# Performance work log

Hardware: AMD Instinct MI355X
Metric: run time of the kernel (lower is better)

## Reference

```python
import jax, jax.numpy as jnp
import numpy as np

S, B, E, H = 2048, 2, 1024, 16
D = E // H  # head_dim = 64


def setup_inputs() -> dict:
    key = jax.random.key(0)
    ks = jax.random.split(key, 5)
    sp = (2.0 / (E + E)) ** 0.5  # xavier-ish scale
    return {
        "x": jax.random.normal(ks[0], (S, B, E), dtype=jnp.float32),
        "wq": jax.random.normal(ks[1], (E, E), dtype=jnp.float32) * sp,
        "bq": jnp.zeros((E,), jnp.float32),
        "wk": jax.random.normal(ks[2], (E, E), dtype=jnp.float32) * sp,
        "bk": jnp.zeros((E,), jnp.float32),
        "wv": jax.random.normal(ks[3], (E, E), dtype=jnp.float32) * sp,
        "bv": jnp.zeros((E,), jnp.float32),
        "wo": jax.random.normal(ks[4], (E, E), dtype=jnp.float32) * sp,
        "bo": jnp.zeros((E,), jnp.float32),
    }


def reference(x, wq, bq, wk, bk, wv, bv, wo, bo):
    # x: (S, B, E), weights in torch Linear convention (out, in)
    scaling = jnp.float32(D ** -0.5)
    q = (jnp.einsum('ibe,fe->ibf', x, wq) + bq) * scaling
    k = jnp.einsum('ibe,fe->ibf', x, wk) + bk
    v = jnp.einsum('ibe,fe->ibf', x, wv) + bv
    q = q.reshape(S, B, H, D)
    k = k.reshape(S, B, H, D)
    v = v.reshape(S, B, H, D)
    # energy: (B, H, S_q, S_k)
    energy = jnp.einsum('ibnf,jbnf->bnij', q, k)
    causal = jnp.triu(jnp.ones((S, S), dtype=bool), k=1)  # True above diagonal
    energy = jnp.where(causal[None, None], -jnp.inf, energy)
    weights = jax.nn.softmax(energy, axis=-1)
    head_ctx = jnp.einsum('bnij,jbnf->ibnf', weights, v)
    context = head_ctx.reshape(S, B, E)
    out = jnp.einsum('ibe,fe->ibf', context, wo) + bo
    return out
```

## Files before the change

### kernel.cpp

```cpp
#include <hip/hip_runtime.h>
#include <hip/hip_bf16.h>
#include <stdint.h>

#define S_LEN 2048
#define BATCH 2
#define EMB   1024
#define NH    16
#define HD    64
#define LOG2E 1.4426950408889634f

typedef __bf16 bf16x8 __attribute__((ext_vector_type(8)));
typedef float  f32x4  __attribute__((ext_vector_type(4)));
typedef unsigned short ushort8 __attribute__((ext_vector_type(8)));

__device__ __forceinline__ unsigned short f2bf(float f) {
  __bf16 h = (__bf16)f;
  return __builtin_bit_cast(unsigned short, h);
}

__device__ __forceinline__ ushort8 cvt8(const float4 a, const float4 b) {
  ushort8 o;
  o[0]=f2bf(a.x); o[1]=f2bf(a.y); o[2]=f2bf(a.z); o[3]=f2bf(a.w);
  o[4]=f2bf(b.x); o[5]=f2bf(b.y); o[6]=f2bf(b.z); o[7]=f2bf(b.w);
  return o;
}

__device__ __forceinline__ uint2 pack4(const f32x4 v) {
  uint2 r;
  r.x = (unsigned)f2bf(v[0]) | ((unsigned)f2bf(v[1]) << 16);
  r.y = (unsigned)f2bf(v[2]) | ((unsigned)f2bf(v[3]) << 16);
  return r;
}

#define GLOAD16(g, l) __builtin_amdgcn_global_load_lds( \
    (const __attribute__((address_space(1))) void*)(g),  \
    (__attribute__((address_space(3))) void*)(l), 16, 0, 0)

__global__ __launch_bounds__(256) void k_cvt(const float* __restrict__ src,
                                             unsigned short* __restrict__ dst,
                                             int n) {
  int i = (blockIdx.x*256 + threadIdx.x)*8;
  if (i >= n) return;
  const float4* s4 = (const float4*)(src + i);
  *(ushort8*)(dst + i) = cvt8(s4[0], s4[1]);
}

__global__ __launch_bounds__(256) void k_cvt_all(
    const float* __restrict__ x,
    const float* __restrict__ wq, const float* __restrict__ wk,
    const float* __restrict__ wv, const float* __restrict__ wo,
    unsigned short* __restrict__ xb, unsigned short* __restrict__ wb,
    unsigned short* __restrict__ wob) {
  const int b = blockIdx.x;
  const float* src;
  unsigned short* dst;
  int off;
  if (b < 2048) { src = x; dst = xb; off = b; }
  else {
    const int t = b - 2048;
    const int z = t >> 9;
    if (z < 3) { src = (z==0) ? wq : ((z==1) ? wk : wv); dst = wb + (size_t)z*EMB*EMB; }
    else       { src = wo; dst = wob; }
    off = t & 511;
  }
  const int i = (off*256 + threadIdx.x)*8;
  const float4* s4 = (const float4*)(src + i);
  *(ushort8*)(dst + i) = cvt8(s4[0], s4[1]);
}

__global__ __launch_bounds__(256) void k_qkv_bb(
    const unsigned short* __restrict__ xb,
    const unsigned short* __restrict__ wb,
    const float* __restrict__ bq, const float* __restrict__ bk,
    const float* __restrict__ bv,
    unsigned short* __restrict__ Qb, unsigned short* __restrict__ Kb,
    unsigned short* __restrict__ Vtb)
{
  __shared__ unsigned short SB[16896];

  const int tid = threadIdx.x;
  const int lin  = blockIdx.x;
  const int wgid = (lin & 7)*96 + (lin >> 3);
  const int mb   = wgid / 24;
  const int t    = wgid % 24;
  const int z    = t >> 3;
  const int nb   = t & 7;
  const int m0 = mb * 128;
  const int n0 = nb * 128;
  const int w = tid >> 6, lane = tid & 63;
  const int wr = w >> 1, wc = w & 1;
  const int lr = lane & 15, lhi = lane >> 4;
  const unsigned short* wz = wb + (size_t)z * (EMB*EMB);

  const unsigned short* ag[2];
  const unsigned short* bg[2];
  int ub[2];
#pragma unroll
  for (int j=0;j<2;++j) {
    const int c    = j*256 + tid;
    const int line = c >> 3;
    const int sp   = (c & 7) ^ (line & 7);
    const int row  = line*2 + (sp >> 2);
    const int q    = sp & 3;
    ag[j] = xb + (size_t)(m0+row)*EMB + q*8;
    bg[j] = wz + (size_t)(n0+row)*EMB + q*8;
    ub[j] = (j*256 + (tid & 192)) * 16;
  }

  auto STAGE = [&](int k0, int b2) {
#pragma unroll
    for (int j=0;j<2;++j) {
      GLOAD16(ag[j] + k0, (char*)(SB + b2*4096)        + ub[j]);
      GLOAD16(bg[j] + k0, (char*)(SB + 8192 + b2*4096) + ub[j]);
    }
  };

  const int asl  = (((lr & 1) << 2) + lhi) ^ (lr >> 1);
  const int rb   = (lr >> 1)*128 + asl*16;
  const int abase = wr*4096 + rb;
  const int bbase = wc*4096 + rb;

  f32x4 acc[4][4];
#pragma unroll
  for (int m=0;m<4;++m)
#pragma unroll
    for (int n=0;n<4;++n) acc[m][n] = (f32x4){0.f,0.f,0.f,0.f};

  STAGE(0, 0);
  int bbuf = 0;
  for (int k0 = 0; k0 < EMB; k0 += 32) {
    if (k0 + 32 < EMB) {
      STAGE(k0 + 32, bbuf^1);
      asm volatile("s_waitcnt vmcnt(4)" ::: "memory");
    } else {
      asm volatile("s_waitcnt vmcnt(0)" ::: "memory");
    }
    __builtin_amdgcn_s_barrier();

    const char* Ab = (const char*)(SB + bbuf*4096);
    const char* Bb = (const char*)(SB + 8192 + bbuf*4096);
    bf16x8 af[4], bfr[4];
#pragma unroll
    for (int m=0;m<4;++m) af[m]  = *(const bf16x8*)(Ab + abase + m*1024);
#pragma unroll
    for (int n=0;n<4;++n) bfr[n] = *(const bf16x8*)(Bb + bbase + n*1024);
    __builtin_amdgcn_s_setprio(1);
#pragma unroll
    for (int m=0;m<4;++m)
#pragma unroll
      for (int n=0;n<4;++n)
        acc[m][n] = __builtin_amdgcn_mfma_f32_16x16x32_bf16(af[m], bfr[n], acc[m][n], 0,0,0);
    __builtin_amdgcn_s_setprio(0);

    __builtin_amdgcn_s_barrier();
    bbuf ^= 1;
  }

  if (z == 2) {
    unsigned short* T = SB;
#pragma unroll
    for (int m=0;m<4;++m)
#pragma unroll
      for (int n=0;n<4;++n) {
        const int fl = wc*64 + n*16 + lr;
        const int i0 = wr*32 + m*8 + lhi*2;
        const float b = bv[n0 + fl];
        const unsigned w0 = (unsigned)f2bf(acc[m][n][0] + b)
                          | ((unsigned)f2bf(acc[m][n][2] + b) << 16);
        const unsigned w1 = (unsigned)f2bf(acc[m][n][1] + b)
                          | ((unsigned)f2bf(acc[m][n][3] + b) << 16);
        *(unsigned*)&T[fl*66 + i0]        = w0;
        *(unsigned*)&T[8448 + fl*66 + i0] = w1;
      }
    __builtin_amdgcn_s_barrier();
    const int h = n0 >> 6;
#pragma unroll
    for (int it = 0; it < 8; ++it) {
      const int jj   = it*256 + tid;
      const int bsel = jj >> 10;
      const int fl   = (jj >> 3) & 127;
      const int ic   = (jj & 7) * 8;
      const ushort8 vv = *(const ushort8*)&T[bsel*8448 + fl*66 + ic];
      const int hh2 = bsel*NH + h + (fl >> 6);
      const int d   = fl & 63;
      *(ushort8*)&Vtb[((size_t)hh2*HD + d)*S_LEN + (m0 >> 1) + ic] = vv;
    }
  } else {
    const float scale = (z==0) ? 0.125f*LOG2E : 1.0f;
    const float* bias = (z==0) ? bq : bk;
    unsigned short* qk = (z==0) ? Qb : Kb;
#pragma unroll
    for (int m=0;m<4;++m)
#pragma unroll
      for (int n=0;n<4;++n)
#pragma unroll
        for (int r=0;r<4;++r) {
          const int rr   = m0 + wr*64 + m*16 + lhi*4 + r;
          const int fcol = n0 + wc*64 + n*16 + lr;
          const float v = (acc[m][n][r] + bias[fcol]) * scale;
          const unsigned short ov = f2bf(v);
          const int i = rr >> 1, bsel = rr & 1;
          const int h = fcol >> 6, d = fcol & 63;
          const int hh = bsel*NH + h;
          qk[((size_t)hh*S_LEN + i)*HD + d] = ov;
        }
  }
}

__global__ __launch_bounds__(256) void k_qkv_bf(
    const unsigned short* __restrict__ xb,
    const float* __restrict__ wq, const float* __restrict__ wk,
    const float* __restrict__ wv,
    const float* __restrict__ bq, const float* __restrict__ bk,
    const float* __restrict__ bv,
    unsigned short* __restrict__ Qb, unsigned short* __restrict__ Kb,
    unsigned short* __restrict__ Vtb)
{
  __shared__ unsigned short Al[128*32];
  __shared__ unsigned short Bl[128*32];
  const int tid = threadIdx.x;
  const int lin  = blockIdx.x;
  const int wgid = (lin & 7)*96 + (lin >> 3);
  const int mb   = wgid / 24;
  const int t    = wgid % 24;
  const int z    = t >> 3;
  const int nb   = t & 7;
  const int m0 = mb * 128;
  const int n0 = nb * 128;
  const int w = tid >> 6, lane = tid & 63;
  const int wr = w >> 1, wc = w & 1;
  const int lr = lane & 15, lhi = lane >> 4;
  const float* wz = (z==0) ? wq : ((z==1) ? wk : wv);

  f32x4 acc[4][4];
#pragma unroll
  for (int m=0;m<4;++m)
#pragma unroll
    for (int n=0;n<4;++n) acc[m][n] = (f32x4){0.f,0.f,0.f,0.f};

  for (int k0 = 0; k0 < EMB; k0 += 32) {
    float4 b0[2], b1[2];
#pragma unroll
    for (int j = 0; j < 2; ++j) {
      const int c   = j*256 + tid;
      const int row = c >> 2;
      const int col = (c & 3) << 3;
      const float* bp = wz + (size_t)(n0+row)*EMB + k0 + col;
      b0[j] = *(const float4*)bp;  b1[j] = *(const float4*)(bp+4);
    }
    __syncthreads();
#pragma unroll
    for (int j = 0; j < 2; ++j) {
      const int c   = j*256 + tid;
      const int row = c >> 2;
      const int col = (c & 3) << 3;
      const int ub  = (j*256 + (tid & 192)) * 16;
      GLOAD16(xb + (size_t)(m0+row)*EMB + k0 + col, (char*)Al + ub);
      *(ushort8*)&Bl[row*32 + col] = cvt8(b0[j], b1[j]);
    }
    __syncthreads();
    bf16x8 af[4], bfr[4];
#pragma unroll
    for (int m=0;m<4;++m) af[m]  = *(const bf16x8*)&Al[(wr*64 + m*16 + lr)*32 + lhi*8];
#pragma unroll
    for (int n=0;n<4;++n) bfr[n] = *(const bf16x8*)&Bl[(wc*64 + n*16 + lr)*32 + lhi*8];
#pragma unroll
    for (int m=0;m<4;++m)
#pragma unroll
      for (int n=0;n<4;++n)
        acc[m][n] = __builtin_amdgcn_mfma_f32_16x16x32_bf16(af[m], bfr[n], acc[m][n], 0,0,0);
  }

  const float scale = (z==0) ? 0.125f*LOG2E : 1.0f;
  const float* bias = (z==0) ? bq : ((z==1) ? bk : bv);
#pragma unroll
  for (int m=0;m<4;++m)
#pragma unroll
    for (int n=0;n<4;++n)
#pragma unroll
      for (int r=0;r<4;++r) {
        const int rr   = m0 + wr*64 + m*16 + lhi*4 + r;
        const int fcol = n0 + wc*64 + n*16 + lr;
        const float v = (acc[m][n][r] + bias[fcol]) * scale;
        const unsigned short ov = f2bf(v);
        const int i = rr >> 1, bsel = rr & 1;
        const int h = fcol >> 6, d = fcol & 63;
        const int hh = bsel*NH + h;
        if (z == 0)      Qb [((size_t)hh*S_LEN + i)*HD + d] = ov;
        else if (z == 1) Kb [((size_t)hh*S_LEN + i)*HD + d] = ov;
        else             Vtb[((size_t)hh*HD + d)*S_LEN + i] = ov;
      }
}

__global__ __launch_bounds__(256) void k_qkv(
    const float* __restrict__ xA, int a_rs, int ishift,
    const float* __restrict__ wq, const float* __restrict__ wk,
    const float* __restrict__ wv,
    const float* __restrict__ bq, const float* __restrict__ bk,
    const float* __restrict__ bv,
    unsigned short* __restrict__ Qb, unsigned short* __restrict__ Kb,
    unsigned short* __restrict__ Vtb)
{
  __shared__ unsigned short Al[128*32];
  __shared__ unsigned short Bl[128*32];
  const int tid = threadIdx.x;
  const int z  = blockIdx.z;
  const int m0 = blockIdx.x * 128;
  const int n0 = blockIdx.y * 128;
  const int w = tid >> 6, lane = tid & 63;
  const int wr = w >> 1, wc = w & 1;
  const int lr = lane & 15, lhi = lane >> 4;
  const float* wz = (z==0) ? wq : ((z==1) ? wk : wv);

  f32x4 acc[4][4];
#pragma unroll
  for (int m=0;m<4;++m)
#pragma unroll
    for (int n=0;n<4;++n) acc[m][n] = (f32x4){0.f,0.f,0.f,0.f};

  for (int k0 = 0; k0 < EMB; k0 += 32) {
    float4 a0[2], a1[2], b0[2], b1[2];
#pragma unroll
    for (int j = 0; j < 2; ++j) {
      const int c   = j*256 + tid;
      const int row = c >> 2;
      const int col = (c & 3) << 3;
      const float* ap = xA + (size_t)(m0+row)*a_rs + k0 + col;
      const float* bp = wz + (size_t)(n0+row)*EMB + k0 + col;
      a0[j] = *(const float4*)ap;  a1[j] = *(const float4*)(ap+4);
      b0[j] = *(const float4*)bp;  b1[j] = *(const float4*)(bp+4);
    }
    __syncthreads();
#pragma unroll
    for (int j = 0; j < 2; ++j) {
      const int c   = j*256 + tid;
      const int row = c >> 2;
      const int col = (c & 3) << 3;
      *(ushort8*)&Al[row*32 + col] = cvt8(a0[j], a1[j]);
      *(ushort8*)&Bl[row*32 + col] = cvt8(b0[j], b1[j]);
    }
    __syncthreads();
    bf16x8 af[4], bfr[4];
#pragma unroll
    for (int m=0;m<4;++m) af[m]  = *(const bf16x8*)&Al[(wr*64 + m*16 + lr)*32 + lhi*8];
#pragma unroll
    for (int n=0;n<4;++n) bfr[n] = *(const bf16x8*)&Bl[(wc*64 + n*16 + lr)*32 + lhi*8];
#pragma unroll
    for (int m=0;m<4;++m)
#pragma unroll
      for (int n=0;n<4;++n)
        acc[m][n] = __builtin_amdgcn_mfma_f32_16x16x32_bf16(af[m], bfr[n], acc[m][n], 0,0,0);
  }

  const float scale = (z==0) ? 0.125f*LOG2E : 1.0f;
  const float* bias = (z==0) ? bq : ((z==1) ? bk : bv);
  const int bmask = (1 << ishift) - 1;
#pragma unroll
  for (int m=0;m<4;++m)
#pragma unroll
    for (int n=0;n<4;++n)
#pragma unroll
      for (int r=0;r<4;++r) {
        const int rr   = m0 + wr*64 + m*16 + lhi*4 + r;
        const int fcol = n0 + wc*64 + n*16 + lr;
        const float v = (acc[m][n][r] + bias[fcol]) * scale;
        const unsigned short ov = f2bf(v);
        const int i = rr >> ishift, bsel = rr & bmask;
        const int h = fcol >> 6, d = fcol & 63;
        const int hh = bsel*NH + h;
        if (z == 0)      Qb [((size_t)hh*S_LEN + i)*HD + d] = ov;
        else if (z == 1) Kb [((size_t)hh*S_LEN + i)*HD + d] = ov;
        else             Vtb[((size_t)hh*HD + d)*S_LEN + i] = ov;
      }
}

__global__ __launch_bounds__(256,4) void k_attn_u(
    const unsigned short* __restrict__ Q,
    const unsigned short* __restrict__ K,
    const unsigned short* __restrict__ Vt,
    unsigned short* __restrict__ ctx, int bshift, int hsh)
{
  __shared__ unsigned short KL[2][64*64];
  __shared__ unsigned short VL[2][64*64];
  __shared__ unsigned short Pl[4][16*64];

  const int tid = threadIdx.x;
  const int w = tid >> 6, lane = tid & 63;
  const int lr = lane & 15, lhi = lane >> 4;

  const int lin = blockIdx.x;
  const int cc  = lin >> hsh;
  const int chunk = (cc < 16) ? cc : (47 - cc);
  const int hh  = lin & ((1 << hsh) - 1);
  const int q0  = chunk*64 + w*16;

  const unsigned short* Qh = Q  + (size_t)hh*S_LEN*HD;
  const unsigned short* Kh = K  + (size_t)hh*S_LEN*HD;
  const unsigned short* Vh = Vt + (size_t)hh*HD*S_LEN;
  char* Pw = (char*)Pl[w];

  const int xm = (lr & 7) << 4;
  int kvb[2];
#pragma unroll
  for (int kf=0;kf<2;++kf) kvb[kf] = lr*128 + ((kf*64 + lhi*16) ^ xm);
  int pwb[4];
#pragma unroll
  for (int kn=0;kn<4;++kn)
    pwb[kn] = lr*128 + ((kn*32 + lhi*8) ^ xm);

  const unsigned short* kga[2];
  const unsigned short* vga[2];
#pragma unroll
  for (int j=0;j<2;++j) {
    const int c   = j*256 + tid;
    const int row = c >> 3;
    const int sb  = (c*16) ^ ((row & 7) << 4);
    const int el  = (sb & 127) >> 1;
    kga[j] = Kh + (size_t)row*HD + el;
    vga[j] = Vh + (size_t)row*S_LEN + el;
  }
  const int ub0 = (tid & 192) * 16;

  bf16x8 qf[2];
#pragma unroll
  for (int kf=0;kf<2;++kf)
    qf[kf] = *(const bf16x8*)&Qh[(size_t)(q0 + lr)*HD + kf*32 + lhi*8];

  f32x4 o[4];
  float rl = 0.f;
#pragma unroll
  for (int dn=0;dn<4;++dn) o[dn] = (f32x4){0.f,0.f,0.f,0.f};

  const int tmax = chunk + 1;

  auto STAGE = [&](int tt, int bb2) {
#pragma unroll
    for (int j=0;j<2;++j) {
      GLOAD16(kga[j] + (size_t)tt*4096, (char*)KL[bb2] + ub0 + j*4096);
      GLOAD16(vga[j] + (size_t)tt*64,   (char*)VL[bb2] + ub0 + j*4096);
    }
  };

  STAGE(0, 0);
  int bb = 0;
  for (int t = 0; t < tmax; ++t) {
    if (t + 1 < tmax) {
      STAGE(t+1, bb^1);
      asm volatile("s_waitcnt vmcnt(4)" ::: "memory");
    } else {
      asm volatile("s_waitcnt vmcnt(0)" ::: "memory");
    }
    __builtin_amdgcn_s_barrier();

    const int kv0 = t*64;
    const char* KB = (const char*)KL[bb];
    const char* VB = (const char*)VL[bb];

    f32x4 st[4];
#pragma unroll
    for (int kn=0;kn<4;++kn) st[kn] = (f32x4){0.f,0.f,0.f,0.f};

    __builtin_amdgcn_s_setprio(1);
#pragma unroll
    for (int kn=0;kn<4;++kn)
#pragma unroll
      for (int kf=0;kf<2;++kf) {
        const bf16x8 kfr = *(const bf16x8*)(KB + kvb[kf] + kn*2048);
        st[kn] = __builtin_amdgcn_mfma_f32_16x16x32_bf16(kfr, qf[kf], st[kn], 0,0,0);
      }
    __builtin_amdgcn_s_setprio(0);

    if (t == tmax-1) {
      const int q = q0 + lr;
#pragma unroll
      for (int kn=0;kn<4;++kn)
#pragma unroll
        for (int r=0;r<4;++r) {
          const int k = kv0 + kn*16 + lhi*4 + r;
          if (k > q) st[kn][r] = -1.0e30f;
        }
    }

#pragma unroll
    for (int kn=0;kn<4;++kn)
#pragma unroll
      for (int r=0;r<4;++r) {
        const float p = exp2f(st[kn][r]);
        st[kn][r] = p;
        rl += p;
      }

#pragma unroll
    for (int kn=0;kn<4;++kn)
      *(uint2*)(Pw + pwb[kn]) = pack4(st[kn]);

#pragma unroll
    for (int ks=0;ks<2;++ks) {
      const bf16x8 pfr = *(const bf16x8*)(Pw + kvb[ks]);
      __builtin_amdgcn_s_setprio(1);
#pragma unroll
      for (int dn=0;dn<4;++dn) {
        const bf16x8 vf = *(const bf16x8*)(VB + kvb[ks] + dn*2048);
        o[dn] = __builtin_amdgcn_mfma_f32_16x16x32_bf16(vf, pfr, o[dn], 0,0,0);
      }
      __builtin_amdgcn_s_setprio(0);
    }

    __builtin_amdgcn_s_barrier();
    bb ^= 1;
  }

  rl += __shfl_xor(rl, 16);
  rl += __shfl_xor(rl, 32);
  const int h = hh & (NH-1);
  const int badd = hh >> 4;
  const float inv = 1.0f / rl;
  const int q = q0 + lr;
  const size_t trow = ((size_t)q << bshift) + badd;
#pragma unroll
  for (int dn=0;dn<4;++dn) {
    f32x4 ov;
#pragma unroll
    for (int r=0;r<4;++r) ov[r] = o[dn][r]*inv;
    *(uint2*)&ctx[trow*EMB + h*HD + dn*16 + lhi*4] = pack4(ov);
  }
}

__global__ __launch_bounds__(256) void k_oproj_bf(
    const unsigned short* __restrict__ ctxA,
    const unsigned short* __restrict__ wob,
    const float* __restrict__ bo,
    float* __restrict__ out)
{
  __shared__ unsigned short Al[2][128*32];
  __shared__ unsigned short Bl[2][128*32];
  const int tid = threadIdx.x;
  const int m0 = blockIdx.x * 128;
  const int n0 = blockIdx.y * 128;
  const int w = tid >> 6, lane = tid & 63;
  const int wr = w >> 1, wc = w & 1;
  const int lr = lane & 15, lhi = lane >> 4;

  const unsigned short* ag[2];
  const unsigned short* bg[2];
  int ub[2];
#pragma unroll
  for (int j=0;j<2;++j) {
    const int c    = j*256 + tid;
    const int line = c >> 3;
    const int sp   = (c & 7) ^ (line & 7);
    const int row  = line*2 + (sp >> 2);
    const int q    = sp & 3;
    ag[j] = ctxA + (size_t)(m0+row)*EMB + q*8;
    bg[j] = wob  + (size_t)(n0+row)*EMB + q*8;
    ub[j] = (j*256 + (tid & 192)) * 16;
  }

  auto STAGE = [&](int k0, int b2) {
#pragma unroll
    for (int j=0;j<2;++j) {
      GLOAD16(ag[j] + k0, (char*)Al[b2] + ub[j]);
      GLOAD16(bg[j] + k0, (char*)Bl[b2] + ub[j]);
    }
  };

  const int asl  = (((lr & 1) << 2) + lhi) ^ (lr >> 1);
  const int rb   = (lr >> 1)*128 + asl*16;
  const int abase = wr*4096 + rb;
  const int bbase = wc*4096 + rb;

  f32x4 acc[4][4];
#pragma unroll
  for (int m=0;m<4;++m)
#pragma unroll
    for (int n=0;n<4;++n) acc[m][n] = (f32x4){0.f,0.f,0.f,0.f};

  STAGE(0, 0);
  int bbuf = 0;
  for (int k0 = 0; k0 < EMB; k0 += 32) {
    if (k0 + 32 < EMB) {
      STAGE(k0 + 32, bbuf^1);
      asm volatile("s_waitcnt vmcnt(4)" ::: "memory");
    } else {
      asm volatile("s_waitcnt vmcnt(0)" ::: "memory");
    }
    __builtin_amdgcn_s_barrier();

    bf16x8 af[4], bfr[4];
#pragma unroll
    for (int m=0;m<4;++m) af[m]  = *(const bf16x8*)((char*)Al[bbuf] + abase + m*1024);
#pragma unroll
    for (int n=0;n<4;++n) bfr[n] = *(const bf16x8*)((char*)Bl[bbuf] + bbase + n*1024);
    __builtin_amdgcn_s_setprio(1);
#pragma unroll
    for (int m=0;m<4;++m)
#pragma unroll
      for (int n=0;n<4;++n)
        acc[m][n] = __builtin_amdgcn_mfma_f32_16x16x32_bf16(af[m], bfr[n], acc[m][n], 0,0,0);
    __builtin_amdgcn_s_setprio(0);

    __builtin_amdgcn_s_barrier();
    bbuf ^= 1;
  }

#pragma unroll
  for (int m=0;m<4;++m)
#pragma unroll
    for (int n=0;n<4;++n)
#pragma unroll
      for (int r=0;r<4;++r) {
        const int rr   = m0 + wr*64 + m*16 + lhi*4 + r;
        const int fcol = n0 + wc*64 + n*16 + lr;
        out[(size_t)rr*EMB + fcol] = acc[m][n][r] + bo[fcol];
      }
}

__global__ __launch_bounds__(256) void k_oproj(
    const unsigned short* __restrict__ ctxA,
    const float* __restrict__ wo,
    const float* __restrict__ bo,
    float* __restrict__ outb, int orm)
{
  __shared__ unsigned short Al[128*32];
  __shared__ unsigned short Bl[128*32];
  const int tid = threadIdx.x;
  const int m0 = blockIdx.x * 128;
  const int n0 = blockIdx.y * 128;
  const int w = tid >> 6, lane = tid & 63;
  const int wr = w >> 1, wc = w & 1;
  const int lr = lane & 15, lhi = lane >> 4;

  f32x4 acc[4][4];
#pragma unroll
  for (int m=0;m<4;++m)
#pragma unroll
    for (int n=0;n<4;++n) acc[m][n] = (f32x4){0.f,0.f,0.f,0.f};

  for (int k0 = 0; k0 < EMB; k0 += 32) {
    float4 b0[2], b1[2];
#pragma unroll
    for (int j = 0; j < 2; ++j) {
      const int c   = j*256 + tid;
      const int row = c >> 2;
      const int col = (c & 3) << 3;
      const float* bp = wo + (size_t)(n0+row)*EMB + k0 + col;
      b0[j] = *(const float4*)bp;  b1[j] = *(const float4*)(bp+4);
    }
    __syncthreads();
#pragma unroll
    for (int j = 0; j < 2; ++j) {
      const int c   = j*256 + tid;
      const int row = c >> 2;
      const int col = (c & 3) << 3;
      const int ub  = (j*256 + (tid & 192)) * 16;
      GLOAD16(ctxA + (size_t)(m0+row)*EMB + k0 + col, (char*)Al + ub);
      *(ushort8*)&Bl[row*32 + col] = cvt8(b0[j], b1[j]);
    }
    __syncthreads();
    bf16x8 af[4], bfr[4];
#pragma unroll
    for (int m=0;m<4;++m) af[m]  = *(const bf16x8*)&Al[(wr*64 + m*16 + lr)*32 + lhi*8];
#pragma unroll
    for (int n=0;n<4;++n) bfr[n] = *(const bf16x8*)&Bl[(wc*64 + n*16 + lr)*32 + lhi*8];
#pragma unroll
    for (int m=0;m<4;++m)
#pragma unroll
      for (int n=0;n<4;++n)
        acc[m][n] = __builtin_amdgcn_mfma_f32_16x16x32_bf16(af[m], bfr[n], acc[m][n], 0,0,0);
  }

#pragma unroll
  for (int m=0;m<4;++m)
#pragma unroll
    for (int n=0;n<4;++n)
#pragma unroll
      for (int r=0;r<4;++r) {
        const int rr   = m0 + wr*64 + m*16 + lhi*4 + r;
        const int fcol = n0 + wc*64 + n*16 + lr;
        outb[(size_t)rr*orm*EMB + fcol] = acc[m][n][r] + bo[fcol];
      }
}

extern "C" void kernel_launch(void* const* d_in, const int* in_sizes, int n_in,
                              void* d_out, int out_size, void* d_ws, size_t ws_size,
                              hipStream_t stream) {
  const float* x  = (const float*)d_in[0];
  const float* wq = (const float*)d_in[1];
  const float* bq = (const float*)d_in[2];
  const float* wk = (const float*)d_in[3];
  const float* bk = (const float*)d_in[4];
  const float* wv = (const float*)d_in[5];
  const float* bv = (const float*)d_in[6];
  const float* wo = (const float*)d_in[7];
  const float* bo = (const float*)d_in[8];
  float* out = (float*)d_out;

  char* ws = (char*)d_ws;
  const size_t MB = (size_t)1 << 20;

  if (ws_size >= 40*MB) {
    unsigned short* Q   = (unsigned short*)(ws + 0*MB);
    unsigned short* K   = (unsigned short*)(ws + 8*MB);
    unsigned short* Vt  = (unsigned short*)(ws + 16*MB);
    unsigned short* wb  = (unsigned short*)(ws + 24*MB);
    unsigned short* xb  = (unsigned short*)(ws + 30*MB);
    unsigned short* wob = (unsigned short*)(ws + 38*MB);
    unsigned short* cx  = (unsigned short*)(ws + 24*MB);

    k_cvt_all<<<4096, 256, 0, stream>>>(x, wq, wk, wv, wo, xb, wb, wob);
    k_qkv_bb<<<768, 256, 0, stream>>>(xb, wb, bq,bk,bv, Q, K, Vt);
    k_attn_u<<<1024, 256, 0, stream>>>(Q, K, Vt, cx, 1, 5);
    k_oproj_bf<<<dim3(32,8), 256, 0, stream>>>(cx, wob, bo, out);
  } else if (ws_size >= 38*MB) {
    unsigned short* Q   = (unsigned short*)(ws + 0*MB);
    unsigned short* K   = (unsigned short*)(ws + 8*MB);
    unsigned short* Vt  = (unsigned short*)(ws + 16*MB);
    unsigned short* wb  = (unsigned short*)(ws + 24*MB);
    unsigned short* xb  = (unsigned short*)(ws + 30*MB);
    unsigned short* cx  = (unsigned short*)(ws + 24*MB);
    unsigned short* wob = Vt;

    k_cvt_all<<<3584, 256, 0, stream>>>(x, wq, wk, wv, wo, xb, wb, (unsigned short*)0);
    k_qkv_bb<<<768, 256, 0, stream>>>(xb, wb, bq,bk,bv, Q, K, Vt);
    k_attn_u<<<1024, 256, 0, stream>>>(Q, K, Vt, cx, 1, 5);
    k_cvt<<<512, 256, 0, stream>>>(wo, wob, EMB*EMB);
    k_oproj_bf<<<dim3(32,8), 256, 0, stream>>>(cx, wob, bo, out);
  } else if (ws_size >= 32*MB) {
    unsigned short* Q   = (unsigned short*)(ws + 0*MB);
    unsigned short* K   = (unsigned short*)(ws + 8*MB);
    unsigned short* Vt  = (unsigned short*)(ws + 16*MB);
    unsigned short* cx  = (unsigned short*)(ws + 24*MB);
    unsigned short* xb  = cx;
    unsigned short* wob = Vt;

    k_cvt<<<2048, 256, 0, stream>>>(x, xb, (S_LEN*BATCH)*EMB);
    k_qkv_bf<<<768, 256, 0, stream>>>(xb, wq,wk,wv, bq,bk,bv, Q, K, Vt);
    k_attn_u<<<1024, 256, 0, stream>>>(Q, K, Vt, cx, 1, 5);
    k_cvt<<<512, 256, 0, stream>>>(wo, wob, EMB*EMB);
    k_oproj_bf<<<dim3(32,8), 256, 0, stream>>>(cx, wob, bo, out);
  } else {
    unsigned short* Q  = (unsigned short*)(ws + 0*MB);
    unsigned short* K  = (unsigned short*)(ws + 4*MB);
    unsigned short* Vt = (unsigned short*)(ws + 8*MB);
    unsigned short* cx = (unsigned short*)(ws + 12*MB);
    for (int b = 0; b < 2; ++b) {
      k_qkv<<<dim3(16,8,3), 256, 0, stream>>>(x + b*EMB, 2*EMB, 0,
                                              wq,wk,wv, bq,bk,bv, Q,K,Vt);
      k_attn_u<<<512, 256, 0, stream>>>(Q, K, Vt, cx, 0, 4);
      k_oproj<<<dim3(16,8), 256, 0, stream>>>(cx, wo, bo, out + b*EMB, 2);
    }
  }
}
```

Before: 110.3 us.

## Enlarge attention query tile to 128 rows with two 16-row subtiles per wave

Each attention block now handles 128 query rows instead of 64, with every wave computing two 16-row query subtiles. Each K/V fragment read from LDS is reused across both subtiles, and half as many blocks are launched. This reduces K/V global loads and LDS reads per query. In exchange it uses more registers and LDS (launch bounds lowered to 3), and waves past their causal end sit idle on the block barrier.

```diff
diff --git a/kernel.cpp b/kernel.cpp
--- a/kernel.cpp
+++ b/kernel.cpp
@@ -374,7 +374,7 @@
       }
 }
 
-__global__ __launch_bounds__(256,4) void k_attn_u(
+__global__ __launch_bounds__(256,3) void k_attn_u(
     const unsigned short* __restrict__ Q,
     const unsigned short* __restrict__ K,
     const unsigned short* __restrict__ Vt,
@@ -382,7 +382,7 @@
 {
   __shared__ unsigned short KL[2][64*64];
   __shared__ unsigned short VL[2][64*64];
-  __shared__ unsigned short Pl[4][16*64];
+  __shared__ unsigned short Pl[4][32*64];
 
   const int tid = threadIdx.x;
   const int w = tid >> 6, lane = tid & 63;
@@ -390,9 +390,9 @@
 
   const int lin = blockIdx.x;
   const int cc  = lin >> hsh;
-  const int chunk = (cc < 16) ? cc : (47 - cc);
+  const int chunk = (cc < 8) ? cc : (23 - cc);
   const int hh  = lin & ((1 << hsh) - 1);
-  const int q0  = chunk*64 + w*16;
+  const int q0  = chunk*128 + w*32;
 
   const unsigned short* Qh = Q  + (size_t)hh*S_LEN*HD;
   const unsigned short* Kh = K  + (size_t)hh*S_LEN*HD;
@@ -421,17 +421,22 @@
   }
   const int ub0 = (tid & 192) * 16;
 
-  bf16x8 qf[2];
-#pragma unroll
-  for (int kf=0;kf<2;++kf)
-    qf[kf] = *(const bf16x8*)&Qh[(size_t)(q0 + lr)*HD + kf*32 + lhi*8];
-
-  f32x4 o[4];
-  float rl = 0.f;
-#pragma unroll
-  for (int dn=0;dn<4;++dn) o[dn] = (f32x4){0.f,0.f,0.f,0.f};
-
-  const int tmax = chunk + 1;
+  bf16x8 qf[2][2];
+#pragma unroll
+  for (int qm=0;qm<2;++qm)
+#pragma unroll
+    for (int kf=0;kf<2;++kf)
+      qf[qm][kf] = *(const bf16x8*)&Qh[(size_t)(q0 + qm*16 + lr)*HD + kf*32 + lhi*8];
+
+  f32x4 o[4][2];
+  float rl[2] = {0.f, 0.f};
+#pragma unroll
+  for (int dn=0;dn<4;++dn)
+#pragma unroll
+    for (int qm=0;qm<2;++qm) o[dn][qm] = (f32x4){0.f,0.f,0.f,0.f};
+
+  const int wtend = ((q0 + 31) >> 6) + 1;
+  const int tmax  = 2*chunk + 2;
 
   auto STAGE = [&](int tt, int bb2) {
 #pragma unroll
@@ -452,77 +457,98 @@
     }
     __builtin_amdgcn_s_barrier();
 
-    const int kv0 = t*64;
-    const char* KB = (const char*)KL[bb];
-    const char* VB = (const char*)VL[bb];
-
-    f32x4 st[4];
-#pragma unroll
-    for (int kn=0;kn<4;++kn) st[kn] = (f32x4){0.f,0.f,0.f,0.f};
-
-    __builtin_amdgcn_s_setprio(1);
-#pragma unroll
-    for (int kn=0;kn<4;++kn)
-#pragma unroll
-      for (int kf=0;kf<2;++kf) {
-        const bf16x8 kfr = *(const bf16x8*)(KB + kvb[kf] + kn*2048);
-        st[kn] = __builtin_amdgcn_mfma_f32_16x16x32_bf16(kfr, qf[kf], st[kn], 0,0,0);
+    if (t < wtend) {
+      const int kv0 = t*64;
+      const char* KB = (const char*)KL[bb];
+      const char* VB = (const char*)VL[bb];
+
+      f32x4 st[4][2];
+#pragma unroll
+      for (int kn=0;kn<4;++kn)
+#pragma unroll
+        for (int qm=0;qm<2;++qm) st[kn][qm] = (f32x4){0.f,0.f,0.f,0.f};
+
+      __builtin_amdgcn_s_setprio(1);
+#pragma unroll
+      for (int kn=0;kn<4;++kn)
+#pragma unroll
+        for (int kf=0;kf<2;++kf) {
+          const bf16x8 kfr = *(const bf16x8*)(KB + kvb[kf] + kn*2048);
+#pragma unroll
+          for (int qm=0;qm<2;++qm)
+            st[kn][qm] = __builtin_amdgcn_mfma_f32_16x16x32_bf16(kfr, qf[qm][kf], st[kn][qm], 0,0,0);
+        }
+      __builtin_amdgcn_s_setprio(0);
+
+      if (t == wtend-1) {
+#pragma unroll
+        for (int qm=0;qm<2;++qm) {
+          const int q = q0 + qm*16 + lr;
+#pragma unroll
+          for (int kn=0;kn<4;++kn)
+#pragma unroll
+            for (int r=0;r<4;++r) {
+              const int k = kv0 + kn*16 + lhi*4 + r;
+              if (k > q) st[kn][qm][r] = -1.0e30f;
+            }
+        }
       }
-    __builtin_amdgcn_s_setprio(0);
-
-    if (t == tmax-1) {
-      const int q = q0 + lr;
-#pragma unroll
-      for (int kn=0;kn<4;++kn)
-#pragma unroll
-        for (int r=0;r<4;++r) {
-          const int k = kv0 + kn*16 + lhi*4 + r;
-          if (k > q) st[kn][r] = -1.0e30f;
+
+#pragma unroll
+      for (int qm=0;qm<2;++qm)
+#pragma unroll
+        for (int kn=0;kn<4;++kn)
+#pragma unroll
+          for (int r=0;r<4;++r) {
+            const float p = exp2f(st[kn][qm][r]);
+            st[kn][qm][r] = p;
+            rl[qm] += p;
+          }
+
+#pragma unroll
+      for (int qm=0;qm<2;++qm)
+#pragma unroll
+        for (int kn=0;kn<4;++kn)
+          *(uint2*)(Pw + qm*2048 + pwb[kn]) = pack4(st[kn][qm]);
+
+#pragma unroll
+      for (int ks=0;ks<2;++ks) {
+        bf16x8 pfr[2];
+#pragma unroll
+        for (int qm=0;qm<2;++qm)
+          pfr[qm] = *(const bf16x8*)(Pw + qm*2048 + kvb[ks]);
+        __builtin_amdgcn_s_setprio(1);
+#pragma unroll
+        for (int dn=0;dn<4;++dn) {
+          const bf16x8 vf = *(const bf16x8*)(VB + kvb[ks] + dn*2048);
+#pragma unroll
+          for (int qm=0;qm<2;++qm)
+            o[dn][qm] = __builtin_amdgcn_mfma_f32_16x16x32_bf16(vf, pfr[qm], o[dn][qm], 0,0,0);
         }
-    }
-
-#pragma unroll
-    for (int kn=0;kn<4;++kn)
-#pragma unroll
-      for (int r=0;r<4;++r) {
-        const float p = exp2f(st[kn][r]);
-        st[kn][r] = p;
-        rl += p;
+        __builtin_amdgcn_s_setprio(0);
       }
-
-#pragma unroll
-    for (int kn=0;kn<4;++kn)
-      *(uint2*)(Pw + pwb[kn]) = pack4(st[kn]);
-
-#pragma unroll
-    for (int ks=0;ks<2;++ks) {
-      const bf16x8 pfr = *(const bf16x8*)(Pw + kvb[ks]);
-      __builtin_amdgcn_s_setprio(1);
-#pragma unroll
-      for (int dn=0;dn<4;++dn) {
-        const bf16x8 vf = *(const bf16x8*)(VB + kvb[ks] + dn*2048);
-        o[dn] = __builtin_amdgcn_mfma_f32_16x16x32_bf16(vf, pfr, o[dn], 0,0,0);
-      }
-      __builtin_amdgcn_s_setprio(0);
-    }
-
+    }
     __builtin_amdgcn_s_barrier();
     bb ^= 1;
   }
 
-  rl += __shfl_xor(rl, 16);
-  rl += __shfl_xor(rl, 32);
   const int h = hh & (NH-1);
   const int badd = hh >> 4;
-  const float inv = 1.0f / rl;
-  const int q = q0 + lr;
-  const size_t trow = ((size_t)q << bshift) + badd;
-#pragma unroll
-  for (int dn=0;dn<4;++dn) {
-    f32x4 ov;
-#pragma unroll
-    for (int r=0;r<4;++r) ov[r] = o[dn][r]*inv;
-    *(uint2*)&ctx[trow*EMB + h*HD + dn*16 + lhi*4] = pack4(ov);
+#pragma unroll
+  for (int qm=0;qm<2;++qm) {
+    float rlq = rl[qm];
+    rlq += __shfl_xor(rlq, 16);
+    rlq += __shfl_xor(rlq, 32);
+    const float inv = 1.0f / rlq;
+    const int q = q0 + qm*16 + lr;
+    const size_t trow = ((size_t)q << bshift) + badd;
+#pragma unroll
+    for (int dn=0;dn<4;++dn) {
+      f32x4 ov;
+#pragma unroll
+      for (int r=0;r<4;++r) ov[r] = o[dn][qm][r]*inv;
+      *(uint2*)&ctx[trow*EMB + h*HD + dn*16 + lhi*4] = pack4(ov);
+    }
   }
 }
 
@@ -709,7 +735,7 @@
 
     k_cvt_all<<<4096, 256, 0, stream>>>(x, wq, wk, wv, wo, xb, wb, wob);
     k_qkv_bb<<<768, 256, 0, stream>>>(xb, wb, bq,bk,bv, Q, K, Vt);
-    k_attn_u<<<1024, 256, 0, stream>>>(Q, K, Vt, cx, 1, 5);
+    k_attn_u<<<512, 256, 0, stream>>>(Q, K, Vt, cx, 1, 5);
     k_oproj_bf<<<dim3(32,8), 256, 0, stream>>>(cx, wob, bo, out);
   } else if (ws_size >= 38*MB) {
     unsigned short* Q   = (unsigned short*)(ws + 0*MB);
@@ -722,7 +748,7 @@
 
     k_cvt_all<<<3584, 256, 0, stream>>>(x, wq, wk, wv, wo, xb, wb, (unsigned short*)0);
     k_qkv_bb<<<768, 256, 0, stream>>>(xb, wb, bq,bk,bv, Q, K, Vt);
-    k_attn_u<<<1024, 256, 0, stream>>>(Q, K, Vt, cx, 1, 5);
+    k_attn_u<<<512, 256, 0, stream>>>(Q, K, Vt, cx, 1, 5);
     k_cvt<<<512, 256, 0, stream>>>(wo, wob, EMB*EMB);
     k_oproj_bf<<<dim3(32,8), 256, 0, stream>>>(cx, wob, bo, out);
   } else if (ws_size >= 32*MB) {
@@ -735,7 +761,7 @@
 
     k_cvt<<<2048, 256, 0, stream>>>(x, xb, (S_LEN*BATCH)*EMB);
     k_qkv_bf<<<768, 256, 0, stream>>>(xb, wq,wk,wv, bq,bk,bv, Q, K, Vt);
-    k_attn_u<<<1024, 256, 0, stream>>>(Q, K, Vt, cx, 1, 5);
+    k_attn_u<<<512, 256, 0, stream>>>(Q, K, Vt, cx, 1, 5);
     k_cvt<<<512, 256, 0, stream>>>(wo, wob, EMB*EMB);
     k_oproj_bf<<<dim3(32,8), 256, 0, stream>>>(cx, wob, bo, out);
   } else {
@@ -746,7 +772,7 @@
     for (int b = 0; b < 2; ++b) {
       k_qkv<<<dim3(16,8,3), 256, 0, stream>>>(x + b*EMB, 2*EMB, 0,
                                               wq,wk,wv, bq,bk,bv, Q,K,Vt);
-      k_attn_u<<<512, 256, 0, stream>>>(Q, K, Vt, cx, 0, 4);
+      k_attn_u<<<256, 256, 0, stream>>>(Q, K, Vt, cx, 0, 4);
       k_oproj<<<dim3(16,8), 256, 0, stream>>>(cx, wo, bo, out + b*EMB, 2);
     }
   }
```

New measurement: 123.2 us. 11.8% more time.
